# Performance work log

Hardware: AMD Instinct MI355X
Metric: run time of the kernel (lower is better)

## Reference

```python
import jax, jax.numpy as jnp
import numpy as np

DIM = 128
HEADS = 4
HEAD_DIM = DIM // HEADS
WS = (8, 8)
N = WS[0] * WS[1]
B = 4096
SCALE = HEAD_DIM ** -0.5


def _relative_position_index():
    # Swin-style relative position index, [N, N] int
    ch = np.arange(WS[0]); cw = np.arange(WS[1])
    coords = np.stack(np.meshgrid(ch, cw, indexing='ij'))          # [2, ws0, ws1]
    flat = coords.reshape(2, -1)                                    # [2, N]
    rel = flat[:, :, None] - flat[:, None, :]                       # [2, N, N]
    rel = rel.transpose(1, 2, 0)                                    # [N, N, 2]
    rel[:, :, 0] += WS[0] - 1
    rel[:, :, 1] += WS[1] - 1
    rel[:, :, 0] *= 2 * WS[1] - 1
    return jnp.asarray(rel.sum(-1))

REL_IDX = _relative_position_index()


def setup_inputs() -> dict:
    key = jax.random.key(0)
    ks = jax.random.split(key, 16)
    def lin(k, din, dout):
        return jax.random.normal(k, (din, dout), jnp.float32) * (din ** -0.5)
    return {
        'x': jax.random.normal(ks[0], (B, N, DIM), jnp.float32),
        'f': jax.random.normal(ks[1], (B, N, DIM), jnp.float32),
        'wq': lin(ks[2], DIM, DIM), 'bq': jnp.zeros((DIM,), jnp.float32),
        'wkv': lin(ks[3], DIM, 2 * DIM), 'bkv': jnp.zeros((2 * DIM,), jnp.float32),
        'wq_f': lin(ks[4], DIM, DIM), 'bq_f': jnp.zeros((DIM,), jnp.float32),
        'wkv_f': lin(ks[5], DIM, 2 * DIM), 'bkv_f': jnp.zeros((2 * DIM,), jnp.float32),
        'bias_table': jax.random.normal(ks[6], ((2 * WS[0] - 1) * (2 * WS[1] - 1), HEADS), jnp.float32) * 0.02,
        'wproj': lin(ks[7], DIM, DIM), 'bproj': jnp.zeros((DIM,), jnp.float32),
    }


def _qkv(t, wq, bq, wkv, bkv):
    Bn, Nn, C = t.shape
    q = (t @ wq + bq).reshape(Bn, Nn, HEADS, HEAD_DIM).transpose(0, 2, 1, 3)   # [B,H,N,D]
    kv = (t @ wkv + bkv).reshape(Bn, Nn, 2, HEADS, HEAD_DIM).transpose(2, 0, 3, 1, 4)
    return q, kv[0], kv[1]


def reference(x, f, wq, bq, wkv, bkv, wq_f, bq_f, wkv_f, bkv_f, bias_table, wproj, bproj):
    q, k, v = _qkv(x, wq, bq, wkv, bkv)
    attn = jnp.einsum('bhnd,bhmd->bhnm', q * SCALE, k)              # [B,H,N,N]
    q_f, k_f, _ = _qkv(f, wq_f, bq_f, wkv_f, bkv_f)
    attn_f = jnp.einsum('bhnd,bhmd->bhnm', q_f * SCALE, k_f)

    bias = bias_table[REL_IDX.reshape(-1)].reshape(N, N, HEADS)     # gather
    bias = bias.transpose(2, 0, 1)                                   # [H,N,N]
    ratio = attn.shape[-1] // bias.shape[-1]
    if ratio > 1:  # repeat last axis (no-op here since N == ws0*ws1)
        bias = jnp.repeat(bias, ratio, axis=-1)

    attn = (attn + bias[None]) * (attn_f + bias[None])               # joint modulation
    attn = jax.nn.softmax(attn, axis=-1)
    out = jnp.einsum('bhnm,bhmd->bhnd', attn, v)                     # [B,H,N,D]
    out = out.transpose(0, 2, 1, 3).reshape(x.shape[0], N, DIM)
    return out @ wproj + bproj
```

## Files before the change

### kernel.cpp

```cpp
#include <hip/hip_runtime.h>

typedef unsigned short u16;
typedef _Float16  f16x8  __attribute__((ext_vector_type(8)));
typedef _Float16  f16x4  __attribute__((ext_vector_type(4)));
typedef _Float16  f16x2  __attribute__((ext_vector_type(2)));
typedef float     f32x4  __attribute__((ext_vector_type(4)));

#define MFMA_F16(a,b,c)  __builtin_amdgcn_mfma_f32_16x16x32_f16(a,b,c,0,0,0)
#define PKRTZ(a,b) __builtin_bit_cast(f16x2, __builtin_amdgcn_cvt_pkrtz((a),(b)))

#define NTOK 64
#define DIM_ 128
#define SCALE_ 0.17677669529663687f

#define HREG 6784
#define KOFF 2304
#define VOFF 4608
#define SQK  36
#define SP   72
#define SAO  40
#define SVT  68
#define SMEM_U16 27136

#define WS_TAB_F32 49152

__device__ __forceinline__ u16 f2h_u(float x) {
    _Float16 h = (_Float16)x;
    return __builtin_bit_cast(u16, h);
}

__global__ void wja_prep(const float* __restrict__ wq, const float* __restrict__ wkv,
                         const float* __restrict__ wq_f, const float* __restrict__ wkv_f,
                         const float* __restrict__ wproj, const float* __restrict__ btab,
                         u16* __restrict__ ws)
{
    const int blk = blockIdx.x;
    const int l = threadIdx.x;
    if (blk < 192) {
        const float* W; int ldw, colbase;
        if (blk < 32)       { W = wq;    ldw = 128; colbase = (blk      >> 2) * 16; }
        else if (blk < 96)  { W = wkv;   ldw = 256; colbase = ((blk- 32) >> 2) * 16; }
        else if (blk < 128) { W = wq_f;  ldw = 128; colbase = ((blk- 96) >> 2) * 16; }
        else if (blk < 160) { W = wkv_f; ldw = 256; colbase = ((blk-128) >> 2) * 16; }
        else                { W = wproj; ldw = 128; colbase = ((blk-160) >> 2) * 16; }
        const int ks = blk & 3;
        const int m = l & 15, g = l >> 4;
        u16* dst = ws + blk * 512 + l * 8;
        #pragma unroll
        for (int i = 0; i < 8; ++i)
            dst[i] = f2h_u(W[(size_t)(32*ks + 8*g + i) * ldw + colbase + m]);
    } else {
        const int h = blk - 192;
        float* tab = (float*)ws + WS_TAB_F32 + h * 4096;
        for (int e = l; e < 4096; e += 64) {
            int i  = e & 3;
            int cc = (e >> 2) & 15;
            int g  = (e >> 6) & 3;
            int nt = (e >> 8) & 3;
            int mt = (e >> 10) & 3;
            int r = 16*mt + 4*g + i;
            int j = 16*nt + cc;
            int idx = ((r >> 3) - (j >> 3) + 7) * 15 + ((r & 7) - (j & 7) + 7);
            tab[e] = btab[idx * 4 + h];
        }
    }
}

__global__ __launch_bounds__(256, 2)
void wja_fused(
    const float* __restrict__ x, const float* __restrict__ f,
    const float* __restrict__ bq, const float* __restrict__ bkv,
    const float* __restrict__ bq_f, const float* __restrict__ bkv_f,
    const float* __restrict__ bproj,
    const u16* __restrict__ ws, float* __restrict__ out)
{
    __shared__ __align__(16) u16 smem[SMEM_U16];
    const int b    = blockIdx.x;
    const int tid  = threadIdx.x;
    const int w    = tid >> 6;
    const int lane = tid & 63;
    const int g    = lane >> 4;
    const int c    = lane & 15;
    const f32x4 zf4 = {0.f, 0.f, 0.f, 0.f};

    u16* const hb = smem + w * HREG;
    const float* const tabw = (const float*)ws + WS_TAB_F32 + w * 4096;

    const float* const xb = x + (size_t)b * (NTOK * DIM_);
    const float* const fb = f + (size_t)b * (NTOK * DIM_);

    auto ldf16 = [](const float* p) -> f16x8 {
        f32x4 v0 = *(const f32x4*)p;
        f32x4 v1 = *(const f32x4*)(p + 4);
        struct Q { f16x2 a, b, c, d; } t;
        t.a = PKRTZ(v0[0], v0[1]);
        t.b = PKRTZ(v0[2], v0[3]);
        t.c = PKRTZ(v1[0], v1[1]);
        t.d = PKRTZ(v1[2], v1[3]);
        return __builtin_bit_cast(f16x8, t);
    };
    auto ldlds8 = [](const u16* p) -> f16x8 {
        struct P2 { f16x4 lo, hi; } t;
        t.lo = *(const f16x4*)p;
        t.hi = *(const f16x4*)(p + 4);
        return __builtin_bit_cast(f16x8, t);
    };
    auto btile = [&](int mt, int nt) -> f32x4 {
        return *(const f32x4*)(tabw + ((mt*4 + nt)*4 + g)*64 + c*4);
    };

    f16x8 xfr[4], ffr[4];
    #pragma unroll
    for (int ks = 0; ks < 4; ++ks) {
        xfr[ks] = ldf16(xb + (16*w + c) * DIM_ + 32*ks + 8*g);
        ffr[ks] = ldf16(fb + (16*w + c) * DIM_ + 32*ks + 8*g);
    }

    auto gemmA = [&](const f16x8* afr, int wbase, const float* biasv, int which) {
        #pragma unroll
        for (int lct = 0; lct < 8; ++lct) {
            f32x4 acc = zf4;
            #pragma unroll
            for (int ks = 0; ks < 4; ++ks) {
                f16x8 bfr = *(const f16x8*)(ws + (wbase + 4*lct + ks) * 512 + lane * 8);
                acc = MFMA_F16(afr[ks], bfr, acc);
            }
            float bv = biasv[16*lct + c];
            const int hh = lct >> 1;
            const int cc = ((lct & 1) << 4) + c;
            if (which == 2) {
                struct H4 { f16x2 lo, hi; } t;
                t.lo = PKRTZ(acc[0] + bv, acc[1] + bv);
                t.hi = PKRTZ(acc[2] + bv, acc[3] + bv);
                *(f16x4*)(smem + hh*HREG + VOFF + cc*SVT + 16*w + 4*g) =
                    __builtin_bit_cast(f16x4, t);
            } else if (which == 1) {
                #pragma unroll
                for (int i = 0; i < 4; ++i)
                    smem[hh*HREG + KOFF + (16*w + 4*g + i)*SQK + cc] = f2h_u(acc[i] + bv);
            } else {
                #pragma unroll
                for (int i = 0; i < 4; ++i)
                    smem[hh*HREG + (16*w + 4*g + i)*SQK + cc] = f2h_u((acc[i] + bv) * SCALE_);
            }
        }
    };

    gemmA(xfr,   0, bq,        0);
    gemmA(xfr,  32, bkv,       1);
    gemmA(xfr,  64, bkv + 128, 2);
    __syncthreads();

    f32x4 S[4][4];
    {
        f16x8 qfr[4], kfr[4];
        #pragma unroll
        for (int t = 0; t < 4; ++t) {
            qfr[t] = ldlds8(hb + (16*t + c) * SQK + 8*g);
            kfr[t] = ldlds8(hb + KOFF + (16*t + c) * SQK + 8*g);
        }
        #pragma unroll
        for (int mt = 0; mt < 4; ++mt)
            #pragma unroll
            for (int nt = 0; nt < 4; ++nt)
                S[mt][nt] = MFMA_F16(qfr[mt], kfr[nt], btile(mt, nt));
    }
    __syncthreads();

    gemmA(ffr,  96, bq_f,  0);
    gemmA(ffr, 128, bkv_f, 1);
    __syncthreads();

    {
        f16x8 kfr[4];
        #pragma unroll
        for (int t = 0; t < 4; ++t)
            kfr[t] = ldlds8(hb + KOFF + (16*t + c) * SQK + 8*g);
        #pragma unroll
        for (int mt = 0; mt < 4; ++mt) {
            f16x8 qfr = ldlds8(hb + (16*mt + c) * SQK + 8*g);
            #pragma unroll
            for (int nt = 0; nt < 4; ++nt) {
                f32x4 sf = MFMA_F16(qfr, kfr[nt], btile(mt, nt));
                #pragma unroll
                for (int i = 0; i < 4; ++i)
                    S[mt][nt][i] *= sf[i];
            }
        }
    }

    float rinv[4][4];
    #pragma unroll
    for (int mt = 0; mt < 4; ++mt)
        #pragma unroll
        for (int i = 0; i < 4; ++i) {
            float m = fmaxf(fmaxf(S[mt][0][i], S[mt][1][i]), fmaxf(S[mt][2][i], S[mt][3][i]));
            #pragma unroll
            for (int d = 1; d < 16; d <<= 1) m = fmaxf(m, __shfl_xor(m, d));
            float s0 = 0.f;
            #pragma unroll
            for (int nt = 0; nt < 4; ++nt) {
                float e = __expf(S[mt][nt][i] - m);
                S[mt][nt][i] = e;
                s0 += e;
            }
            #pragma unroll
            for (int d = 1; d < 16; d <<= 1) s0 += __shfl_xor(s0, d);
            rinv[mt][i] = __builtin_amdgcn_rcpf(s0);
        }

    #pragma unroll
    for (int mt = 0; mt < 4; ++mt)
        #pragma unroll
        for (int nt = 0; nt < 4; ++nt)
            #pragma unroll
            for (int i = 0; i < 4; ++i)
                hb[(16*mt + 4*g + i) * SP + 16*nt + c] = f2h_u(S[mt][nt][i]);

    f32x4 O[4][2] = { { zf4, zf4 }, { zf4, zf4 }, { zf4, zf4 }, { zf4, zf4 } };
    #pragma unroll
    for (int ks = 0; ks < 2; ++ks) {
        f16x8 pfr[4], vfr[2];
        #pragma unroll
        for (int mt = 0; mt < 4; ++mt)
            pfr[mt] = *(const f16x8*)(hb + (16*mt + c) * SP + 32*ks + 8*g);
        #pragma unroll
        for (int nt = 0; nt < 2; ++nt)
            vfr[nt] = ldlds8(hb + VOFF + (16*nt + c) * SVT + 32*ks + 8*g);
        #pragma unroll
        for (int mt = 0; mt < 4; ++mt)
            #pragma unroll
            for (int nt = 0; nt < 2; ++nt)
                O[mt][nt] = MFMA_F16(pfr[mt], vfr[nt], O[mt][nt]);
    }

    #pragma unroll
    for (int mt = 0; mt < 4; ++mt)
        #pragma unroll
        for (int nt = 0; nt < 2; ++nt)
            #pragma unroll
            for (int i = 0; i < 4; ++i)
                hb[(16*mt + 4*g + i) * SAO + 16*nt + c] = f2h_u(O[mt][nt][i] * rinv[mt][i]);

    __syncthreads();

    f32x4 PO[4][2] = { { zf4, zf4 }, { zf4, zf4 }, { zf4, zf4 }, { zf4, zf4 } };
    #pragma unroll
    for (int ks = 0; ks < 4; ++ks) {
        const u16* ao = smem + ks * HREG;
        f16x8 afr[4];
        #pragma unroll
        for (int mt = 0; mt < 4; ++mt)
            afr[mt] = *(const f16x8*)(ao + (16*mt + c) * SAO + 8*g);
        #pragma unroll
        for (int lct = 0; lct < 2; ++lct) {
            f16x8 bfr = *(const f16x8*)(ws + (160 + (2*w + lct) * 4 + ks) * 512 + lane * 8);
            #pragma unroll
            for (int mt = 0; mt < 4; ++mt)
                PO[mt][lct] = MFMA_F16(afr[mt], bfr, PO[mt][lct]);
        }
    }

    float* const ob = out + (size_t)b * 8192;
    #pragma unroll
    for (int lct = 0; lct < 2; ++lct) {
        float bv = bproj[32*w + 16*lct + c];
        #pragma unroll
        for (int mt = 0; mt < 4; ++mt)
            #pragma unroll
            for (int i = 0; i < 4; ++i)
                ob[(16*mt + 4*g + i) * 128 + 32*w + 16*lct + c] = PO[mt][lct][i] + bv;
    }
}

extern "C" void kernel_launch(void* const* d_in, const int* in_sizes, int n_in,
                              void* d_out, int out_size, void* d_ws, size_t ws_size,
                              hipStream_t stream)
{
    const float* x     = (const float*)d_in[0];
    const float* f     = (const float*)d_in[1];
    const float* wq    = (const float*)d_in[2];
    const float* bq    = (const float*)d_in[3];
    const float* wkv   = (const float*)d_in[4];
    const float* bkv   = (const float*)d_in[5];
    const float* wq_f  = (const float*)d_in[6];
    const float* bq_f  = (const float*)d_in[7];
    const float* wkv_f = (const float*)d_in[8];
    const float* bkv_f = (const float*)d_in[9];
    const float* btab  = (const float*)d_in[10];
    const float* wproj = (const float*)d_in[11];
    const float* bproj = (const float*)d_in[12];
    u16* ws    = (u16*)d_ws;
    float* out = (float*)d_out;

    hipLaunchKernelGGL(wja_prep, dim3(196), dim3(64), 0, stream,
                       wq, wkv, wq_f, wkv_f, wproj, btab, ws);
    hipLaunchKernelGGL(wja_fused, dim3(4096), dim3(256), 0, stream,
                       x, f, bq, bkv, bq_f, bkv_f, bproj, ws, out);
}
```

Before: 185.2 us.

## Assign each wave its own head in QKV projection to drop block barriers

The QKV projection GEMMs are re-partitioned so each wave computes all 64 token rows for one head's 32 columns instead of 16 rows across all heads. Each wave then writes only its own head region in shared memory and reads it back itself, so the block-wide barriers between the projection and attention phases are removed. In exchange each wave loads the full x and f tiles (16 fragments each) from global memory, which raises register pressure and redundant global reads by a factor of four.

```diff
diff --git a/kernel.cpp b/kernel.cpp
--- a/kernel.cpp
+++ b/kernel.cpp
@@ -109,47 +109,61 @@
         return *(const f32x4*)(tabw + ((mt*4 + nt)*4 + g)*64 + c*4);
     };
 
-    f16x8 xfr[4], ffr[4];
-    #pragma unroll
-    for (int ks = 0; ks < 4; ++ks) {
-        xfr[ks] = ldf16(xb + (16*w + c) * DIM_ + 32*ks + 8*g);
-        ffr[ks] = ldf16(fb + (16*w + c) * DIM_ + 32*ks + 8*g);
-    }
-
-    auto gemmA = [&](const f16x8* afr, int wbase, const float* biasv, int which) {
-        #pragma unroll
-        for (int lct = 0; lct < 8; ++lct) {
-            f32x4 acc = zf4;
+    auto gemmA = [&](const f16x8* afr, int fragbase, const float* biasv, int which) {
+        #pragma unroll
+        for (int lct = 0; lct < 2; ++lct) {
+            f32x4 acc[4] = { zf4, zf4, zf4, zf4 };
             #pragma unroll
             for (int ks = 0; ks < 4; ++ks) {
-                f16x8 bfr = *(const f16x8*)(ws + (wbase + 4*lct + ks) * 512 + lane * 8);
-                acc = MFMA_F16(afr[ks], bfr, acc);
+                f16x8 bfr = *(const f16x8*)(ws + (fragbase + lct*4 + ks) * 512 + lane * 8);
+                #pragma unroll
+                for (int mt = 0; mt < 4; ++mt)
+                    acc[mt] = MFMA_F16(afr[mt*4+ks], bfr, acc[mt]);
             }
-            float bv = biasv[16*lct + c];
-            const int hh = lct >> 1;
-            const int cc = ((lct & 1) << 4) + c;
+            float bv = biasv[lct*16 + c];
+            const int cc = (lct << 4) + c;
             if (which == 2) {
-                struct H4 { f16x2 lo, hi; } t;
-                t.lo = PKRTZ(acc[0] + bv, acc[1] + bv);
-                t.hi = PKRTZ(acc[2] + bv, acc[3] + bv);
-                *(f16x4*)(smem + hh*HREG + VOFF + cc*SVT + 16*w + 4*g) =
-                    __builtin_bit_cast(f16x4, t);
+                #pragma unroll
+                for (int mt = 0; mt < 4; ++mt) {
+                    struct H4 { f16x2 lo, hi; } t;
+                    t.lo = PKRTZ(acc[mt][0] + bv, acc[mt][1] + bv);
+                    t.hi = PKRTZ(acc[mt][2] + bv, acc[mt][3] + bv);
+                    *(f16x4*)(hb + VOFF + cc*SVT + 16*mt + 4*g) =
+                        __builtin_bit_cast(f16x4, t);
+                }
             } else if (which == 1) {
                 #pragma unroll
-                for (int i = 0; i < 4; ++i)
-                    smem[hh*HREG + KOFF + (16*w + 4*g + i)*SQK + cc] = f2h_u(acc[i] + bv);
+                for (int mt = 0; mt < 4; ++mt)
+                    #pragma unroll
+                    for (int i = 0; i < 4; ++i)
+                        hb[KOFF + (16*mt + 4*g + i)*SQK + cc] = f2h_u(acc[mt][i] + bv);
             } else {
                 #pragma unroll
-                for (int i = 0; i < 4; ++i)
-                    smem[hh*HREG + (16*w + 4*g + i)*SQK + cc] = f2h_u((acc[i] + bv) * SCALE_);
+                for (int mt = 0; mt < 4; ++mt)
+                    #pragma unroll
+                    for (int i = 0; i < 4; ++i)
+                        hb[(16*mt + 4*g + i)*SQK + cc] = f2h_u((acc[mt][i] + bv) * SCALE_);
             }
         }
     };
 
-    gemmA(xfr,   0, bq,        0);
-    gemmA(xfr,  32, bkv,       1);
-    gemmA(xfr,  64, bkv + 128, 2);
-    __syncthreads();
+    f16x8 xfr[16];
+    #pragma unroll
+    for (int mt = 0; mt < 4; ++mt)
+        #pragma unroll
+        for (int ks = 0; ks < 4; ++ks)
+            xfr[mt*4+ks] = ldf16(xb + (16*mt + c) * DIM_ + 32*ks + 8*g);
+
+    gemmA(xfr,   0 + 8*w, bq        + 32*w, 0);
+    gemmA(xfr,  32 + 8*w, bkv       + 32*w, 1);
+    gemmA(xfr,  64 + 8*w, bkv + 128 + 32*w, 2);
+
+    f16x8 ffr[16];
+    #pragma unroll
+    for (int mt = 0; mt < 4; ++mt)
+        #pragma unroll
+        for (int ks = 0; ks < 4; ++ks)
+            ffr[mt*4+ks] = ldf16(fb + (16*mt + c) * DIM_ + 32*ks + 8*g);
 
     f32x4 S[4][4];
     {
@@ -165,11 +179,9 @@
             for (int nt = 0; nt < 4; ++nt)
                 S[mt][nt] = MFMA_F16(qfr[mt], kfr[nt], btile(mt, nt));
     }
-    __syncthreads();
-
-    gemmA(ffr,  96, bq_f,  0);
-    gemmA(ffr, 128, bkv_f, 1);
-    __syncthreads();
+
+    gemmA(ffr,  96 + 8*w, bq_f  + 32*w, 0);
+    gemmA(ffr, 128 + 8*w, bkv_f + 32*w, 1);
 
     {
         f16x8 kfr[4];
```

Result: slower. 240.2 us (+29.7%).
